# Kernel optimization log

Hardware: AMD Instinct MI355X
Metric: run time of the kernel (lower is better)

The kernel has to match this reference:

```python
import jax, jax.numpy as jnp
import numpy as np

BINS = 10


def setup_inputs() -> dict:
    key = jax.random.key(0)
    k1, k2 = jax.random.split(key)
    x = jax.random.uniform(k1, (16384, 2048), dtype=jnp.float32, minval=1e-4, maxval=1.0 - 1e-4)
    target = jax.random.uniform(k2, (16384, 2048), dtype=jnp.float32)
    return {"x": x, "target": target}


def reference(x, target):
    # gradient magnitude (detached in original)
    g = jnp.abs(jax.lax.stop_gradient(x) - target)
    # _g2bin: floor(g * (bins - 0.0001)) -> integer bin ids in [0, BINS-1]
    bin_idx = jnp.floor(g * (BINS - 1e-4)).astype(jnp.int32)
    # histogram (replaces the serialized per-bin python loop)
    bin_count = jnp.bincount(bin_idx.ravel(), length=BINS).astype(jnp.float32)
    N = x.shape[0] * x.shape[1]
    nonempty_bins = jnp.sum(bin_count > 0).astype(jnp.float32)
    gd = jnp.clip(bin_count * nonempty_bins, 1.0, None)
    beta = N / gd  # [BINS]
    # BCE on probabilities, reweighted by gathered beta
    loss = -(target * jnp.log(x) + (1.0 - target) * jnp.log(1.0 - x))
    loss = loss * beta[bin_idx]
    return jnp.mean(loss)
```

## Files before the change

### kernel.cpp

```cpp
#include <hip/hip_runtime.h>

#define BINS 10

__device__ __forceinline__ void accum_elem(float xx, float tt,
                                           float* __restrict__ sum,
                                           unsigned* __restrict__ cnt) {
    float g = fabsf(xx - tt);
    int b = (int)(g * 9.9999f);
    b = b > (BINS - 1) ? (BINS - 1) : b;
    float loss = -(tt * __logf(xx) + (1.0f - tt) * __logf(1.0f - xx));
#pragma unroll
    for (int k = 0; k < BINS; ++k) {
        bool m = (b == k);
        sum[k] += m ? loss : 0.0f;
        cnt[k] += m ? 1u : 0u;
    }
}

template <bool ATOMIC>
__global__ __launch_bounds__(256) void ghm_partial(
    const float* __restrict__ x, const float* __restrict__ t,
    float* __restrict__ psum, unsigned* __restrict__ pcnt,
    int n4, long long n_total)
{
    float sum[BINS];
    unsigned cnt[BINS];
#pragma unroll
    for (int k = 0; k < BINS; ++k) { sum[k] = 0.0f; cnt[k] = 0u; }

    const float4* __restrict__ x4 = (const float4*)x;
    const float4* __restrict__ t4 = (const float4*)t;
    int tid = blockIdx.x * blockDim.x + threadIdx.x;
    int stride = gridDim.x * blockDim.x;

    int i = tid;
    for (; i + stride < n4; i += 2 * stride) {
        float4 xa = x4[i];
        float4 ta = t4[i];
        float4 xb = x4[i + stride];
        float4 tb = t4[i + stride];
        accum_elem(xa.x, ta.x, sum, cnt);
        accum_elem(xa.y, ta.y, sum, cnt);
        accum_elem(xa.z, ta.z, sum, cnt);
        accum_elem(xa.w, ta.w, sum, cnt);
        accum_elem(xb.x, tb.x, sum, cnt);
        accum_elem(xb.y, tb.y, sum, cnt);
        accum_elem(xb.z, tb.z, sum, cnt);
        accum_elem(xb.w, tb.w, sum, cnt);
    }
    if (i < n4) {
        float4 xa = x4[i];
        float4 ta = t4[i];
        accum_elem(xa.x, ta.x, sum, cnt);
        accum_elem(xa.y, ta.y, sum, cnt);
        accum_elem(xa.z, ta.z, sum, cnt);
        accum_elem(xa.w, ta.w, sum, cnt);
    }
    long long tail_base = (long long)n4 * 4;
    long long rem = n_total - tail_base;
    if ((long long)tid < rem) {
        accum_elem(x[tail_base + tid], t[tail_base + tid], sum, cnt);
    }

#pragma unroll
    for (int k = 0; k < BINS; ++k) {
#pragma unroll
        for (int off = 32; off > 0; off >>= 1) {
            sum[k] += __shfl_down(sum[k], off, 64);
            cnt[k] += (unsigned)__shfl_down((int)cnt[k], off, 64);
        }
    }

    __shared__ float s_sum[4][BINS];
    __shared__ unsigned s_cnt[4][BINS];
    int lane = threadIdx.x & 63;
    int wv = threadIdx.x >> 6;
    if (lane == 0) {
#pragma unroll
        for (int k = 0; k < BINS; ++k) { s_sum[wv][k] = sum[k]; s_cnt[wv][k] = cnt[k]; }
    }
    __syncthreads();
    if (threadIdx.x < BINS) {
        float s = 0.0f;
        unsigned c = 0u;
#pragma unroll
        for (int w = 0; w < 4; ++w) { s += s_sum[w][threadIdx.x]; c += s_cnt[w][threadIdx.x]; }
        if (ATOMIC) {
            atomicAdd(&psum[threadIdx.x], s);
            atomicAdd(&pcnt[threadIdx.x], c);
        } else {
            psum[(size_t)blockIdx.x * BINS + threadIdx.x] = s;
            pcnt[(size_t)blockIdx.x * BINS + threadIdx.x] = c;
        }
    }
}

__global__ void ghm_zero(float* psum, unsigned* pcnt) {
    if (threadIdx.x < BINS) { psum[threadIdx.x] = 0.0f; pcnt[threadIdx.x] = 0u; }
}

__global__ __launch_bounds__(256) void ghm_final(
    const float* __restrict__ psum, const unsigned* __restrict__ pcnt,
    float* __restrict__ out, int nblocks, float Nf)
{
    float sum[BINS];
    unsigned cnt[BINS];
#pragma unroll
    for (int k = 0; k < BINS; ++k) { sum[k] = 0.0f; cnt[k] = 0u; }

    for (int i = threadIdx.x; i < nblocks; i += blockDim.x) {
#pragma unroll
        for (int k = 0; k < BINS; ++k) {
            sum[k] += psum[(size_t)i * BINS + k];
            cnt[k] += pcnt[(size_t)i * BINS + k];
        }
    }

#pragma unroll
    for (int k = 0; k < BINS; ++k) {
#pragma unroll
        for (int off = 32; off > 0; off >>= 1) {
            sum[k] += __shfl_down(sum[k], off, 64);
            cnt[k] += (unsigned)__shfl_down((int)cnt[k], off, 64);
        }
    }

    __shared__ float s_sum[4][BINS];
    __shared__ unsigned s_cnt[4][BINS];
    int lane = threadIdx.x & 63;
    int wv = threadIdx.x >> 6;
    if (lane == 0) {
#pragma unroll
        for (int k = 0; k < BINS; ++k) { s_sum[wv][k] = sum[k]; s_cnt[wv][k] = cnt[k]; }
    }
    __syncthreads();

    if (threadIdx.x == 0) {
        float tot_s[BINS];
        unsigned tot_c[BINS];
#pragma unroll
        for (int k = 0; k < BINS; ++k) {
            float s = 0.0f;
            unsigned c = 0u;
#pragma unroll
            for (int w = 0; w < 4; ++w) { s += s_sum[w][k]; c += s_cnt[w][k]; }
            tot_s[k] = s;
            tot_c[k] = c;
        }
        float nonempty = 0.0f;
#pragma unroll
        for (int k = 0; k < BINS; ++k) nonempty += (tot_c[k] > 0u) ? 1.0f : 0.0f;
        float total = 0.0f;
#pragma unroll
        for (int k = 0; k < BINS; ++k) {
            float gd = (float)tot_c[k] * nonempty;
            gd = gd < 1.0f ? 1.0f : gd;
            float beta = Nf / gd;
            total += tot_s[k] * beta;
        }
        out[0] = total / Nf;
    }
}

extern "C" void kernel_launch(void* const* d_in, const int* in_sizes, int n_in,
                              void* d_out, int out_size, void* d_ws, size_t ws_size,
                              hipStream_t stream) {
    const float* x = (const float*)d_in[0];
    const float* t = (const float*)d_in[1];
    float* out = (float*)d_out;

    long long N = (long long)in_sizes[0];
    int n4 = (int)(N / 4);

    const int nblocks = 2048;
    const size_t per_block = (size_t)BINS * (sizeof(float) + sizeof(unsigned));

    if (ws_size >= (size_t)nblocks * per_block) {
        float* psum = (float*)d_ws;
        unsigned* pcnt = (unsigned*)(psum + (size_t)nblocks * BINS);
        ghm_partial<false><<<nblocks, 256, 0, stream>>>(x, t, psum, pcnt, n4, N);
        ghm_final<<<1, 256, 0, stream>>>(psum, pcnt, out, nblocks, (float)N);
    } else {
        float* psum = (float*)d_ws;
        unsigned* pcnt = (unsigned*)(psum + BINS);
        ghm_zero<<<1, 64, 0, stream>>>(psum, pcnt);
        ghm_partial<true><<<nblocks, 256, 0, stream>>>(x, t, psum, pcnt, n4, N);
        ghm_final<<<1, 256, 0, stream>>>(psum, pcnt, out, 1, (float)N);
    }
}
```

Before: 290.7 us.

## Split into histogram pass with ballot counts and beta-weighted loss sum pass

Replaces the single pass that kept 10 per-bin loss sums and counts per thread with two passes. The first computes bin counts using wave ballots and popcounts; the second applies the precomputed negative betas from shared memory to a single scalar accumulator. This removes most of the per-element select/add work across bins, at the cost of reading both inputs twice and launching extra kernels.

```diff
diff --git a/kernel.cpp b/kernel.cpp
--- a/kernel.cpp
+++ b/kernel.cpp
@@ -2,31 +2,26 @@
 
 #define BINS 10
 
-__device__ __forceinline__ void accum_elem(float xx, float tt,
-                                           float* __restrict__ sum,
-                                           unsigned* __restrict__ cnt) {
+__device__ __forceinline__ int bin_of(float xx, float tt) {
     float g = fabsf(xx - tt);
     int b = (int)(g * 9.9999f);
-    b = b > (BINS - 1) ? (BINS - 1) : b;
-    float loss = -(tt * __logf(xx) + (1.0f - tt) * __logf(1.0f - xx));
-#pragma unroll
-    for (int k = 0; k < BINS; ++k) {
-        bool m = (b == k);
-        sum[k] += m ? loss : 0.0f;
-        cnt[k] += m ? 1u : 0u;
-    }
+    return b > (BINS - 1) ? (BINS - 1) : b;
+}
+
+__device__ __forceinline__ void count_elem(int b, unsigned* __restrict__ wc) {
+#pragma unroll
+    for (int k = 0; k < BINS; ++k)
+        wc[k] += (unsigned)__popcll(__ballot(b == k));
 }
 
 template <bool ATOMIC>
-__global__ __launch_bounds__(256) void ghm_partial(
+__global__ __launch_bounds__(256) void ghm_count(
     const float* __restrict__ x, const float* __restrict__ t,
-    float* __restrict__ psum, unsigned* __restrict__ pcnt,
-    int n4, long long n_total)
-{
-    float sum[BINS];
-    unsigned cnt[BINS];
-#pragma unroll
-    for (int k = 0; k < BINS; ++k) { sum[k] = 0.0f; cnt[k] = 0u; }
+    unsigned* __restrict__ pcnt, int n4, long long n_total)
+{
+    unsigned wc[BINS];
+#pragma unroll
+    for (int k = 0; k < BINS; ++k) wc[k] = 0u;
 
     const float4* __restrict__ x4 = (const float4*)x;
     const float4* __restrict__ t4 = (const float4*)t;
@@ -39,127 +34,177 @@
         float4 ta = t4[i];
         float4 xb = x4[i + stride];
         float4 tb = t4[i + stride];
-        accum_elem(xa.x, ta.x, sum, cnt);
-        accum_elem(xa.y, ta.y, sum, cnt);
-        accum_elem(xa.z, ta.z, sum, cnt);
-        accum_elem(xa.w, ta.w, sum, cnt);
-        accum_elem(xb.x, tb.x, sum, cnt);
-        accum_elem(xb.y, tb.y, sum, cnt);
-        accum_elem(xb.z, tb.z, sum, cnt);
-        accum_elem(xb.w, tb.w, sum, cnt);
+        count_elem(bin_of(xa.x, ta.x), wc);
+        count_elem(bin_of(xa.y, ta.y), wc);
+        count_elem(bin_of(xa.z, ta.z), wc);
+        count_elem(bin_of(xa.w, ta.w), wc);
+        count_elem(bin_of(xb.x, tb.x), wc);
+        count_elem(bin_of(xb.y, tb.y), wc);
+        count_elem(bin_of(xb.z, tb.z), wc);
+        count_elem(bin_of(xb.w, tb.w), wc);
     }
     if (i < n4) {
         float4 xa = x4[i];
         float4 ta = t4[i];
-        accum_elem(xa.x, ta.x, sum, cnt);
-        accum_elem(xa.y, ta.y, sum, cnt);
-        accum_elem(xa.z, ta.z, sum, cnt);
-        accum_elem(xa.w, ta.w, sum, cnt);
+        count_elem(bin_of(xa.x, ta.x), wc);
+        count_elem(bin_of(xa.y, ta.y), wc);
+        count_elem(bin_of(xa.z, ta.z), wc);
+        count_elem(bin_of(xa.w, ta.w), wc);
     }
     long long tail_base = (long long)n4 * 4;
     long long rem = n_total - tail_base;
     if ((long long)tid < rem) {
-        accum_elem(x[tail_base + tid], t[tail_base + tid], sum, cnt);
-    }
-
+        count_elem(bin_of(x[tail_base + tid], t[tail_base + tid]), wc);
+    }
+
+    __shared__ unsigned s_c[4][BINS];
+    int lane = threadIdx.x & 63;
+    int wv = threadIdx.x >> 6;
+    if (lane == 0) {
+#pragma unroll
+        for (int k = 0; k < BINS; ++k) s_c[wv][k] = wc[k];
+    }
+    __syncthreads();
+    if (threadIdx.x < BINS) {
+        unsigned c = s_c[0][threadIdx.x] + s_c[1][threadIdx.x]
+                   + s_c[2][threadIdx.x] + s_c[3][threadIdx.x];
+        if (ATOMIC) atomicAdd(&pcnt[threadIdx.x], c);
+        else        pcnt[(size_t)blockIdx.x * BINS + threadIdx.x] = c;
+    }
+}
+
+__global__ __launch_bounds__(256) void ghm_beta(
+    const unsigned* __restrict__ pcnt, float* __restrict__ nbeta,
+    int nblocks, float Nf)
+{
+    unsigned cnt[BINS];
+#pragma unroll
+    for (int k = 0; k < BINS; ++k) cnt[k] = 0u;
+
+    for (int i = threadIdx.x; i < nblocks; i += blockDim.x) {
+#pragma unroll
+        for (int k = 0; k < BINS; ++k) cnt[k] += pcnt[(size_t)i * BINS + k];
+    }
 #pragma unroll
     for (int k = 0; k < BINS; ++k) {
 #pragma unroll
-        for (int off = 32; off > 0; off >>= 1) {
-            sum[k] += __shfl_down(sum[k], off, 64);
+        for (int off = 32; off > 0; off >>= 1)
             cnt[k] += (unsigned)__shfl_down((int)cnt[k], off, 64);
+    }
+    __shared__ unsigned s_c[4][BINS];
+    int lane = threadIdx.x & 63;
+    int wv = threadIdx.x >> 6;
+    if (lane == 0) {
+#pragma unroll
+        for (int k = 0; k < BINS; ++k) s_c[wv][k] = cnt[k];
+    }
+    __syncthreads();
+    if (threadIdx.x == 0) {
+        unsigned tot[BINS];
+        float nonempty = 0.0f;
+#pragma unroll
+        for (int k = 0; k < BINS; ++k) {
+            tot[k] = s_c[0][k] + s_c[1][k] + s_c[2][k] + s_c[3][k];
+            nonempty += (tot[k] > 0u) ? 1.0f : 0.0f;
         }
-    }
-
-    __shared__ float s_sum[4][BINS];
-    __shared__ unsigned s_cnt[4][BINS];
-    int lane = threadIdx.x & 63;
-    int wv = threadIdx.x >> 6;
-    if (lane == 0) {
-#pragma unroll
-        for (int k = 0; k < BINS; ++k) { s_sum[wv][k] = sum[k]; s_cnt[wv][k] = cnt[k]; }
-    }
-    __syncthreads();
-    if (threadIdx.x < BINS) {
-        float s = 0.0f;
-        unsigned c = 0u;
-#pragma unroll
-        for (int w = 0; w < 4; ++w) { s += s_sum[w][threadIdx.x]; c += s_cnt[w][threadIdx.x]; }
-        if (ATOMIC) {
-            atomicAdd(&psum[threadIdx.x], s);
-            atomicAdd(&pcnt[threadIdx.x], c);
-        } else {
-            psum[(size_t)blockIdx.x * BINS + threadIdx.x] = s;
-            pcnt[(size_t)blockIdx.x * BINS + threadIdx.x] = c;
+#pragma unroll
+        for (int k = 0; k < BINS; ++k) {
+            float gd = (float)tot[k] * nonempty;
+            gd = gd < 1.0f ? 1.0f : gd;
+            nbeta[k] = -(Nf / gd);
         }
     }
 }
 
-__global__ void ghm_zero(float* psum, unsigned* pcnt) {
-    if (threadIdx.x < BINS) { psum[threadIdx.x] = 0.0f; pcnt[threadIdx.x] = 0u; }
-}
-
-__global__ __launch_bounds__(256) void ghm_final(
-    const float* __restrict__ psum, const unsigned* __restrict__ pcnt,
-    float* __restrict__ out, int nblocks, float Nf)
-{
-    float sum[BINS];
-    unsigned cnt[BINS];
-#pragma unroll
-    for (int k = 0; k < BINS; ++k) { sum[k] = 0.0f; cnt[k] = 0u; }
-
-    for (int i = threadIdx.x; i < nblocks; i += blockDim.x) {
-#pragma unroll
-        for (int k = 0; k < BINS; ++k) {
-            sum[k] += psum[(size_t)i * BINS + k];
-            cnt[k] += pcnt[(size_t)i * BINS + k];
-        }
-    }
-
-#pragma unroll
-    for (int k = 0; k < BINS; ++k) {
-#pragma unroll
-        for (int off = 32; off > 0; off >>= 1) {
-            sum[k] += __shfl_down(sum[k], off, 64);
-            cnt[k] += (unsigned)__shfl_down((int)cnt[k], off, 64);
-        }
-    }
-
-    __shared__ float s_sum[4][BINS];
-    __shared__ unsigned s_cnt[4][BINS];
-    int lane = threadIdx.x & 63;
-    int wv = threadIdx.x >> 6;
-    if (lane == 0) {
-#pragma unroll
-        for (int k = 0; k < BINS; ++k) { s_sum[wv][k] = sum[k]; s_cnt[wv][k] = cnt[k]; }
-    }
-    __syncthreads();
-
+__device__ __forceinline__ float welem(float xx, float tt,
+                                       const float* __restrict__ s_nb) {
+    int b = bin_of(xx, tt);
+    float p = tt * __logf(xx) + (1.0f - tt) * __logf(1.0f - xx);
+    return p * s_nb[b];
+}
+
+template <bool ATOMIC>
+__global__ __launch_bounds__(256) void ghm_wsum(
+    const float* __restrict__ x, const float* __restrict__ t,
+    const float* __restrict__ nbeta, float* __restrict__ psum,
+    int n4, long long n_total)
+{
+    __shared__ float s_nb[BINS];
+    if (threadIdx.x < BINS) s_nb[threadIdx.x] = nbeta[threadIdx.x];
+    __syncthreads();
+
+    const float4* __restrict__ x4 = (const float4*)x;
+    const float4* __restrict__ t4 = (const float4*)t;
+    int tid = blockIdx.x * blockDim.x + threadIdx.x;
+    int stride = gridDim.x * blockDim.x;
+
+    float acc = 0.0f;
+    int i = tid;
+    for (; i + stride < n4; i += 2 * stride) {
+        float4 xa = x4[i];
+        float4 ta = t4[i];
+        float4 xb = x4[i + stride];
+        float4 tb = t4[i + stride];
+        acc += welem(xa.x, ta.x, s_nb);
+        acc += welem(xa.y, ta.y, s_nb);
+        acc += welem(xa.z, ta.z, s_nb);
+        acc += welem(xa.w, ta.w, s_nb);
+        acc += welem(xb.x, tb.x, s_nb);
+        acc += welem(xb.y, tb.y, s_nb);
+        acc += welem(xb.z, tb.z, s_nb);
+        acc += welem(xb.w, tb.w, s_nb);
+    }
+    if (i < n4) {
+        float4 xa = x4[i];
+        float4 ta = t4[i];
+        acc += welem(xa.x, ta.x, s_nb);
+        acc += welem(xa.y, ta.y, s_nb);
+        acc += welem(xa.z, ta.z, s_nb);
+        acc += welem(xa.w, ta.w, s_nb);
+    }
+    long long tail_base = (long long)n4 * 4;
+    long long rem = n_total - tail_base;
+    if ((long long)tid < rem) {
+        acc += welem(x[tail_base + tid], t[tail_base + tid], s_nb);
+    }
+
+#pragma unroll
+    for (int off = 32; off > 0; off >>= 1)
+        acc += __shfl_down(acc, off, 64);
+
+    __shared__ float s_s[4];
+    int lane = threadIdx.x & 63;
+    int wv = threadIdx.x >> 6;
+    if (lane == 0) s_s[wv] = acc;
+    __syncthreads();
     if (threadIdx.x == 0) {
-        float tot_s[BINS];
-        unsigned tot_c[BINS];
-#pragma unroll
-        for (int k = 0; k < BINS; ++k) {
-            float s = 0.0f;
-            unsigned c = 0u;
-#pragma unroll
-            for (int w = 0; w < 4; ++w) { s += s_sum[w][k]; c += s_cnt[w][k]; }
-            tot_s[k] = s;
-            tot_c[k] = c;
-        }
-        float nonempty = 0.0f;
-#pragma unroll
-        for (int k = 0; k < BINS; ++k) nonempty += (tot_c[k] > 0u) ? 1.0f : 0.0f;
-        float total = 0.0f;
-#pragma unroll
-        for (int k = 0; k < BINS; ++k) {
-            float gd = (float)tot_c[k] * nonempty;
-            gd = gd < 1.0f ? 1.0f : gd;
-            float beta = Nf / gd;
-            total += tot_s[k] * beta;
-        }
-        out[0] = total / Nf;
-    }
+        float bs = s_s[0] + s_s[1] + s_s[2] + s_s[3];
+        if (ATOMIC) atomicAdd(psum, bs);
+        else        psum[blockIdx.x] = bs;
+    }
+}
+
+__global__ void ghm_zero(unsigned* pcnt, float* psum) {
+    if (threadIdx.x < BINS) pcnt[threadIdx.x] = 0u;
+    if (threadIdx.x == 0) psum[0] = 0.0f;
+}
+
+__global__ __launch_bounds__(256) void ghm_finish(
+    const float* __restrict__ psum, float* __restrict__ out,
+    int nblocks, float Nf)
+{
+    float s = 0.0f;
+    for (int i = threadIdx.x; i < nblocks; i += blockDim.x) s += psum[i];
+#pragma unroll
+    for (int off = 32; off > 0; off >>= 1)
+        s += __shfl_down(s, off, 64);
+    __shared__ float s_s[4];
+    int lane = threadIdx.x & 63;
+    int wv = threadIdx.x >> 6;
+    if (lane == 0) s_s[wv] = s;
+    __syncthreads();
+    if (threadIdx.x == 0)
+        out[0] = (s_s[0] + s_s[1] + s_s[2] + s_s[3]) / Nf;
 }
 
 extern "C" void kernel_launch(void* const* d_in, const int* in_sizes, int n_in,
@@ -171,20 +216,29 @@
 
     long long N = (long long)in_sizes[0];
     int n4 = (int)(N / 4);
-
-    const int nblocks = 2048;
-    const size_t per_block = (size_t)BINS * (sizeof(float) + sizeof(unsigned));
-
-    if (ws_size >= (size_t)nblocks * per_block) {
-        float* psum = (float*)d_ws;
-        unsigned* pcnt = (unsigned*)(psum + (size_t)nblocks * BINS);
-        ghm_partial<false><<<nblocks, 256, 0, stream>>>(x, t, psum, pcnt, n4, N);
-        ghm_final<<<1, 256, 0, stream>>>(psum, pcnt, out, nblocks, (float)N);
+    const int nb = 2048;
+    float Nf = (float)N;
+
+    size_t need = (size_t)nb * BINS * sizeof(unsigned)
+                + (size_t)BINS * sizeof(float)
+                + (size_t)nb * sizeof(float);
+
+    if (ws_size >= need) {
+        unsigned* pcnt = (unsigned*)d_ws;
+        float* nbeta = (float*)(pcnt + (size_t)nb * BINS);
+        float* psum = nbeta + BINS;
+        ghm_count<false><<<nb, 256, 0, stream>>>(x, t, pcnt, n4, N);
+        ghm_beta<<<1, 256, 0, stream>>>(pcnt, nbeta, nb, Nf);
+        ghm_wsum<false><<<nb, 256, 0, stream>>>(x, t, nbeta, psum, n4, N);
+        ghm_finish<<<1, 256, 0, stream>>>(psum, out, nb, Nf);
     } else {
-        float* psum = (float*)d_ws;
-        unsigned* pcnt = (unsigned*)(psum + BINS);
-        ghm_zero<<<1, 64, 0, stream>>>(psum, pcnt);
-        ghm_partial<true><<<nblocks, 256, 0, stream>>>(x, t, psum, pcnt, n4, N);
-        ghm_final<<<1, 256, 0, stream>>>(psum, pcnt, out, 1, (float)N);
-    }
-}
+        unsigned* pcnt = (unsigned*)d_ws;
+        float* nbeta = (float*)(pcnt + BINS);
+        float* psum = nbeta + BINS;
+        ghm_zero<<<1, 64, 0, stream>>>(pcnt, psum);
+        ghm_count<true><<<nb, 256, 0, stream>>>(x, t, pcnt, n4, N);
+        ghm_beta<<<1, 256, 0, stream>>>(pcnt, nbeta, 1, Nf);
+        ghm_wsum<true><<<nb, 256, 0, stream>>>(x, t, nbeta, psum, n4, N);
+        ghm_finish<<<1, 256, 0, stream>>>(psum, out, 1, Nf);
+    }
+}
```

After: 328.9 us. 1.13x slower.

## Add flat one-shot kernel with packed bin counters and bin-major partials

Applied to the files above, without the earlier changes.

Adds a fast path when N is a multiple of 4096. Each block loads 4096 elements up front with no loop. Per-thread bin counts are packed into one 64-bit word (5 bits per bin) to cut the per-element select/add work. Per-block partials are stored bin-major and reduced by a parallel final kernel. The trade-offs are many more blocks and a larger partials buffer in exchange for less ALU work per element and better load parallelism.

```diff
diff --git a/kernel.cpp b/kernel.cpp
--- a/kernel.cpp
+++ b/kernel.cpp
@@ -2,13 +2,150 @@
 
 #define BINS 10
 
-__device__ __forceinline__ void accum_elem(float xx, float tt,
-                                           float* __restrict__ sum,
-                                           unsigned* __restrict__ cnt) {
+__device__ __forceinline__ int bin_of(float xx, float tt) {
     float g = fabsf(xx - tt);
     int b = (int)(g * 9.9999f);
-    b = b > (BINS - 1) ? (BINS - 1) : b;
-    float loss = -(tt * __logf(xx) + (1.0f - tt) * __logf(1.0f - xx));
+    return b > (BINS - 1) ? (BINS - 1) : b;
+}
+
+__device__ __forceinline__ float loss_of(float xx, float tt) {
+    return -(tt * __logf(xx) + (1.0f - tt) * __logf(1.0f - xx));
+}
+
+__device__ __forceinline__ void accum_flat(float xx, float tt,
+                                           float* __restrict__ sum,
+                                           unsigned long long& cpack) {
+    int b = bin_of(xx, tt);
+    float loss = loss_of(xx, tt);
+    cpack += 1ull << (5 * b);
+#pragma unroll
+    for (int k = 0; k < BINS; ++k)
+        sum[k] += (b == k) ? loss : 0.0f;
+}
+
+__global__ __launch_bounds__(256) void ghm_flat(
+    const float4* __restrict__ x4, const float4* __restrict__ t4,
+    float* __restrict__ psum, unsigned* __restrict__ pcnt, int nb)
+{
+    int base = blockIdx.x * 1024 + threadIdx.x;
+
+    float4 xa = x4[base];
+    float4 ta = t4[base];
+    float4 xb = x4[base + 256];
+    float4 tb = t4[base + 256];
+    float4 xc = x4[base + 512];
+    float4 tc = t4[base + 512];
+    float4 xd = x4[base + 768];
+    float4 td = t4[base + 768];
+
+    float sum[BINS];
+#pragma unroll
+    for (int k = 0; k < BINS; ++k) sum[k] = 0.0f;
+    unsigned long long cpack = 0ull;
+
+    accum_flat(xa.x, ta.x, sum, cpack);
+    accum_flat(xa.y, ta.y, sum, cpack);
+    accum_flat(xa.z, ta.z, sum, cpack);
+    accum_flat(xa.w, ta.w, sum, cpack);
+    accum_flat(xb.x, tb.x, sum, cpack);
+    accum_flat(xb.y, tb.y, sum, cpack);
+    accum_flat(xb.z, tb.z, sum, cpack);
+    accum_flat(xb.w, tb.w, sum, cpack);
+    accum_flat(xc.x, tc.x, sum, cpack);
+    accum_flat(xc.y, tc.y, sum, cpack);
+    accum_flat(xc.z, tc.z, sum, cpack);
+    accum_flat(xc.w, tc.w, sum, cpack);
+    accum_flat(xd.x, td.x, sum, cpack);
+    accum_flat(xd.y, td.y, sum, cpack);
+    accum_flat(xd.z, td.z, sum, cpack);
+    accum_flat(xd.w, td.w, sum, cpack);
+
+    unsigned cnt[BINS];
+#pragma unroll
+    for (int k = 0; k < BINS; ++k)
+        cnt[k] = (unsigned)((cpack >> (5 * k)) & 31ull);
+
+#pragma unroll
+    for (int k = 0; k < BINS; ++k) {
+#pragma unroll
+        for (int off = 32; off > 0; off >>= 1) {
+            sum[k] += __shfl_down(sum[k], off, 64);
+            cnt[k] += (unsigned)__shfl_down((int)cnt[k], off, 64);
+        }
+    }
+
+    __shared__ float s_sum[4][BINS];
+    __shared__ unsigned s_cnt[4][BINS];
+    int lane = threadIdx.x & 63;
+    int wv = threadIdx.x >> 6;
+    if (lane == 0) {
+#pragma unroll
+        for (int k = 0; k < BINS; ++k) { s_sum[wv][k] = sum[k]; s_cnt[wv][k] = cnt[k]; }
+    }
+    __syncthreads();
+    if (threadIdx.x < BINS) {
+        float s = 0.0f;
+        unsigned c = 0u;
+#pragma unroll
+        for (int w = 0; w < 4; ++w) { s += s_sum[w][threadIdx.x]; c += s_cnt[w][threadIdx.x]; }
+        psum[(size_t)threadIdx.x * nb + blockIdx.x] = s;
+        pcnt[(size_t)threadIdx.x * nb + blockIdx.x] = c;
+    }
+}
+
+__global__ __launch_bounds__(256) void ghm_final_bm(
+    const float* __restrict__ psum, const unsigned* __restrict__ pcnt,
+    float* __restrict__ out, int nb, float Nf)
+{
+    __shared__ float s_s[4];
+    __shared__ unsigned s_c[4];
+    __shared__ float tot_s[BINS];
+    __shared__ unsigned tot_c[BINS];
+    int lane = threadIdx.x & 63;
+    int wv = threadIdx.x >> 6;
+
+    for (int k = 0; k < BINS; ++k) {
+        float s = 0.0f;
+        unsigned c = 0u;
+        for (int i = threadIdx.x; i < nb; i += 256) {
+            s += psum[(size_t)k * nb + i];
+            c += pcnt[(size_t)k * nb + i];
+        }
+#pragma unroll
+        for (int off = 32; off > 0; off >>= 1) {
+            s += __shfl_down(s, off, 64);
+            c += (unsigned)__shfl_down((int)c, off, 64);
+        }
+        if (lane == 0) { s_s[wv] = s; s_c[wv] = c; }
+        __syncthreads();
+        if (threadIdx.x == 0) {
+            tot_s[k] = s_s[0] + s_s[1] + s_s[2] + s_s[3];
+            tot_c[k] = s_c[0] + s_c[1] + s_c[2] + s_c[3];
+        }
+        __syncthreads();
+    }
+
+    if (threadIdx.x == 0) {
+        float nonempty = 0.0f;
+#pragma unroll
+        for (int k = 0; k < BINS; ++k) nonempty += (tot_c[k] > 0u) ? 1.0f : 0.0f;
+        float total = 0.0f;
+#pragma unroll
+        for (int k = 0; k < BINS; ++k) {
+            float gd = (float)tot_c[k] * nonempty;
+            gd = gd < 1.0f ? 1.0f : gd;
+            float beta = Nf / gd;
+            total += tot_s[k] * beta;
+        }
+        out[0] = total / Nf;
+    }
+}
+
+__device__ __forceinline__ void accum_gen(float xx, float tt,
+                                          float* __restrict__ sum,
+                                          unsigned* __restrict__ cnt) {
+    int b = bin_of(xx, tt);
+    float loss = loss_of(xx, tt);
 #pragma unroll
     for (int k = 0; k < BINS; ++k) {
         bool m = (b == k);
@@ -33,33 +170,18 @@
     int tid = blockIdx.x * blockDim.x + threadIdx.x;
     int stride = gridDim.x * blockDim.x;
 
-    int i = tid;
-    for (; i + stride < n4; i += 2 * stride) {
-        float4 xa = x4[i];
-        float4 ta = t4[i];
-        float4 xb = x4[i + stride];
-        float4 tb = t4[i + stride];
-        accum_elem(xa.x, ta.x, sum, cnt);
-        accum_elem(xa.y, ta.y, sum, cnt);
-        accum_elem(xa.z, ta.z, sum, cnt);
-        accum_elem(xa.w, ta.w, sum, cnt);
-        accum_elem(xb.x, tb.x, sum, cnt);
-        accum_elem(xb.y, tb.y, sum, cnt);
-        accum_elem(xb.z, tb.z, sum, cnt);
-        accum_elem(xb.w, tb.w, sum, cnt);
-    }
-    if (i < n4) {
-        float4 xa = x4[i];
-        float4 ta = t4[i];
-        accum_elem(xa.x, ta.x, sum, cnt);
-        accum_elem(xa.y, ta.y, sum, cnt);
-        accum_elem(xa.z, ta.z, sum, cnt);
-        accum_elem(xa.w, ta.w, sum, cnt);
+    for (int i = tid; i < n4; i += stride) {
+        float4 xv = x4[i];
+        float4 tv = t4[i];
+        accum_gen(xv.x, tv.x, sum, cnt);
+        accum_gen(xv.y, tv.y, sum, cnt);
+        accum_gen(xv.z, tv.z, sum, cnt);
+        accum_gen(xv.w, tv.w, sum, cnt);
     }
     long long tail_base = (long long)n4 * 4;
     long long rem = n_total - tail_base;
     if ((long long)tid < rem) {
-        accum_elem(x[tail_base + tid], t[tail_base + tid], sum, cnt);
+        accum_gen(x[tail_base + tid], t[tail_base + tid], sum, cnt);
     }
 
 #pragma unroll
@@ -171,20 +293,33 @@
 
     long long N = (long long)in_sizes[0];
     int n4 = (int)(N / 4);
+    float Nf = (float)N;
+
+    if (N % 4096 == 0 && N / 4096 <= 0x7fffffffLL) {
+        int nb = (int)(N / 4096);
+        size_t need = (size_t)nb * BINS * (sizeof(float) + sizeof(unsigned));
+        if (ws_size >= need) {
+            float* psum = (float*)d_ws;
+            unsigned* pcnt = (unsigned*)(psum + (size_t)BINS * nb);
+            ghm_flat<<<nb, 256, 0, stream>>>((const float4*)x, (const float4*)t,
+                                             psum, pcnt, nb);
+            ghm_final_bm<<<1, 256, 0, stream>>>(psum, pcnt, out, nb, Nf);
+            return;
+        }
+    }
 
     const int nblocks = 2048;
     const size_t per_block = (size_t)BINS * (sizeof(float) + sizeof(unsigned));
-
     if (ws_size >= (size_t)nblocks * per_block) {
         float* psum = (float*)d_ws;
         unsigned* pcnt = (unsigned*)(psum + (size_t)nblocks * BINS);
         ghm_partial<false><<<nblocks, 256, 0, stream>>>(x, t, psum, pcnt, n4, N);
-        ghm_final<<<1, 256, 0, stream>>>(psum, pcnt, out, nblocks, (float)N);
+        ghm_final<<<1, 256, 0, stream>>>(psum, pcnt, out, nblocks, Nf);
     } else {
         float* psum = (float*)d_ws;
         unsigned* pcnt = (unsigned*)(psum + BINS);
         ghm_zero<<<1, 64, 0, stream>>>(psum, pcnt);
         ghm_partial<true><<<nblocks, 256, 0, stream>>>(x, t, psum, pcnt, n4, N);
-        ghm_final<<<1, 256, 0, stream>>>(psum, pcnt, out, 1, (float)N);
-    }
-}
+        ghm_final<<<1, 256, 0, stream>>>(psum, pcnt, out, 1, Nf);
+    }
+}
```

Result: slower. 364.0 us (+25.2%).
